# Optimization experiments

Hardware: AMD Instinct MI355X
Metric: run time of the kernel (lower is better)

Reference implementation:

```python
import jax, jax.numpy as jnp
import numpy as np

N_VERT = 100000
N_EDGE = 50000
NNZ = 3200000
IN_CH = 256
OUT_CH = 64


def setup_inputs() -> dict:
    key = jax.random.key(0)
    k1, k2, k3, k4, k5, k6 = jax.random.split(key, 6)
    X = jax.random.normal(k1, (N_VERT, IN_CH), dtype=jnp.float32)
    W = jax.random.normal(k2, (OUT_CH, IN_CH), dtype=jnp.float32) * (IN_CH ** -0.5)
    degE = jax.random.uniform(k3, (N_EDGE,), dtype=jnp.float32, minval=0.01, maxval=1.0)
    degV = jax.random.uniform(k4, (N_VERT,), dtype=jnp.float32, minval=0.01, maxval=1.0)
    Wdiag = jnp.ones((N_EDGE,), dtype=jnp.float32)
    v_idx = jax.random.randint(k5, (NNZ,), 0, N_VERT, dtype=jnp.int32)
    e_idx = jax.random.randint(k6, (NNZ,), 0, N_EDGE, dtype=jnp.int32)
    return {"X": X, "W": W, "degE": degE, "degV": degV, "Wdiag": Wdiag,
            "v_idx": v_idx, "e_idx": e_idx}


def reference(X, W, degE, degV, Wdiag, v_idx, e_idx):
    # Dense projection: [N, in] @ [in, out] -> [N, out]
    Xp = jnp.einsum('ni,oi->no', X, W)
    # Stage 1: vertex -> hyperedge aggregation, degE + Wdiag normalization
    Xe = jax.ops.segment_sum(Xp[v_idx], e_idx, num_segments=N_EDGE)
    Xe = Xe * (degE * Wdiag)[:, None]
    # Stage 2: hyperedge -> vertex aggregation, degV normalization
    Xv = jax.ops.segment_sum(Xe[e_idx], v_idx, num_segments=N_VERT)
    Xv = Xv * degV[:, None]
    return Xv
```

## Files before the change

### kernel.cpp

```cpp
#include <hip/hip_runtime.h>

#define NV   100000
#define NE   50000
#define NNZ  3200000
#define KIN  256
#define KOUT 64

#define NB    256
#define CHUNK (NNZ / NB)
#define TS    6250
#define NBE   782
#define NBV   1563
#define NBINS (NBE + NBV)
#define LSCAN (NBINS * NB)
#define NBLK_SCAN ((LSCAN + 1023) / 1024)

#define PROJ_BLKS 196

#define ECAP_E 6144
#define ECAP_V 4096

typedef short short8 __attribute__((ext_vector_type(8)));
typedef float f32x4  __attribute__((ext_vector_type(4)));

__device__ __forceinline__ unsigned short f2bf(float f) {
    union { float f; unsigned u; } c{f};
    const unsigned lsb = (c.u >> 16) & 1u;
    return (unsigned short)((c.u + 0x7FFFu + lsb) >> 16);
}
__device__ __forceinline__ float bf2f_lo(unsigned u) {
    union { unsigned u; float f; } c{u << 16};
    return c.f;
}
__device__ __forceinline__ float bf2f_hi(unsigned u) {
    union { unsigned u; float f; } c{u & 0xFFFF0000u};
    return c.f;
}
__device__ __forceinline__ short8 pack8(const float4 lo, const float4 hi) {
    short8 r;
    r[0] = (short)f2bf(lo.x); r[1] = (short)f2bf(lo.y);
    r[2] = (short)f2bf(lo.z); r[3] = (short)f2bf(lo.w);
    r[4] = (short)f2bf(hi.x); r[5] = (short)f2bf(hi.y);
    r[6] = (short)f2bf(hi.z); r[7] = (short)f2bf(hi.w);
    return r;
}

__global__ __launch_bounds__(256) void k_wb(const float* __restrict__ W,
                                            unsigned short* __restrict__ Wb) {
    const int i = blockIdx.x * 256 + threadIdx.x;
    Wb[i] = f2bf(W[i]);
}

__global__ __launch_bounds__(1024) void k_projhist(const float* __restrict__ X,
                                                   const unsigned short* __restrict__ Wb,
                                                   unsigned short* __restrict__ Xpb,
                                                   const int* __restrict__ v_idx,
                                                   const int* __restrict__ e_idx,
                                                   int* __restrict__ mat) {
    __shared__ int h[NBINS];
    if (blockIdx.x < PROJ_BLKS) {
        const int tid  = threadIdx.x;
        const int lane = tid & 63;
        const int wv   = tid >> 6;
        const int l15  = lane & 15;
        const int l4   = lane >> 4;
        const int rbase = blockIdx.x * 512 + wv * 32;

        const int r0 = min(rbase + l15,      NV - 1);
        const int r1 = min(rbase + 16 + l15, NV - 1);
        const float* xp0 = X + (size_t)r0 * KIN + l4 * 8;
        const float* xp1 = X + (size_t)r1 * KIN + l4 * 8;
        const unsigned short* wp = Wb + (size_t)l15 * KIN + l4 * 8;

        f32x4 acc[2][4];
#pragma unroll
        for (int t = 0; t < 2; ++t)
#pragma unroll
            for (int g = 0; g < 4; ++g)
                acc[t][g] = (f32x4){0.f, 0.f, 0.f, 0.f};

#pragma unroll
        for (int s = 0; s < 8; ++s) {
            const int k0 = s * 32;
            const float4 a0lo = *(const float4*)(xp0 + k0);
            const float4 a0hi = *(const float4*)(xp0 + k0 + 4);
            const float4 a1lo = *(const float4*)(xp1 + k0);
            const float4 a1hi = *(const float4*)(xp1 + k0 + 4);
            short8 b[4];
#pragma unroll
            for (int g = 0; g < 4; ++g)
                b[g] = *(const short8*)(wp + (size_t)g * 16 * KIN + k0);
            const short8 a0 = pack8(a0lo, a0hi);
            const short8 a1 = pack8(a1lo, a1hi);
#pragma unroll
            for (int g = 0; g < 4; ++g) {
                acc[0][g] = __builtin_amdgcn_mfma_f32_16x16x32_bf16(a0, b[g], acc[0][g], 0, 0, 0);
                acc[1][g] = __builtin_amdgcn_mfma_f32_16x16x32_bf16(a1, b[g], acc[1][g], 0, 0, 0);
            }
        }

#pragma unroll
        for (int t = 0; t < 2; ++t)
#pragma unroll
            for (int i = 0; i < 4; ++i) {
                const int r = rbase + t * 16 + l4 * 4 + i;
                if (r < NV) {
#pragma unroll
                    for (int g = 0; g < 4; ++g)
                        Xpb[(size_t)r * KOUT + g * 16 + l15] = f2bf(acc[t][g][i]);
                }
            }
    } else {
        const int bb = blockIdx.x - PROJ_BLKS;
        const int tid = threadIdx.x;
        for (int i = tid; i < NBINS; i += 1024) h[i] = 0;
        __syncthreads();
        const int base = bb * CHUNK;
        for (int i = tid; i < CHUNK; i += 1024) {
            atomicAdd(&h[e_idx[base + i] >> 6], 1);
            atomicAdd(&h[NBE + (v_idx[base + i] >> 6)], 1);
        }
        __syncthreads();
        for (int j = tid; j < NBINS; j += 1024) mat[j * NB + bb] = h[j];
    }
}

__global__ __launch_bounds__(1024) void k_scan1(int* __restrict__ mat,
                                                int* __restrict__ bsum) {
    __shared__ int buf[1024];
    const int tid = threadIdx.x;
    const int i = blockIdx.x * 1024 + tid;
    const int v = (i < LSCAN) ? mat[i] : 0;
    buf[tid] = v;
    __syncthreads();
    for (int d = 1; d < 1024; d <<= 1) {
        int t = (tid >= d) ? buf[tid - d] : 0;
        __syncthreads();
        buf[tid] += t;
        __syncthreads();
    }
    if (i < LSCAN) mat[i] = buf[tid] - v;
    if (tid == 1023) bsum[blockIdx.x] = buf[1023];
}

__global__ __launch_bounds__(1024) void k_scan2(int* __restrict__ bsum) {
    __shared__ int buf[1024];
    const int tid = threadIdx.x;
    const int v = (tid < NBLK_SCAN) ? bsum[tid] : 0;
    buf[tid] = v;
    __syncthreads();
    for (int d = 1; d < 1024; d <<= 1) {
        int t = (tid >= d) ? buf[tid - d] : 0;
        __syncthreads();
        buf[tid] += t;
        __syncthreads();
    }
    if (tid < NBLK_SCAN) bsum[tid] = buf[tid] - v;
}

__global__ __launch_bounds__(1024) void k_scan3(int* __restrict__ mat,
                                                const int* __restrict__ bsum) {
    const int i = blockIdx.x * 1024 + threadIdx.x;
    if (i < LSCAN) mat[i] += bsum[blockIdx.x];
}

__global__ __launch_bounds__(1024) void k_partsort2(const int* __restrict__ v_idx,
                                                    const int* __restrict__ e_idx,
                                                    const int* __restrict__ mat,
                                                    unsigned* __restrict__ partE,
                                                    unsigned* __restrict__ partV) {
    __shared__ unsigned sbuf[TS];
    __shared__ unsigned short binbuf[TS];
    __shared__ int hist[NBV], pfx[NBV], cur[NBV], gdst[NBV];
    const int side = (blockIdx.x >= NB) ? 1 : 0;
    const int b = blockIdx.x - side * NB;
    const int tid = threadIdx.x;
    const int nbin = side ? NBV : NBE;
    const int rowOff = side ? NBE : 0;
    const int sub    = side ? NNZ : 0;
    unsigned* __restrict__ part = side ? partV : partE;

    for (int j = tid; j < nbin; j += 1024)
        gdst[j] = mat[(rowOff + j) * NB + b] - sub;

    const int base = b * CHUNK;
    for (int tile = 0; tile < CHUNK / TS; ++tile) {
        __syncthreads();
        for (int j = tid; j < nbin; j += 1024) hist[j] = 0;
        __syncthreads();

        int sb[7]; unsigned svv[7];
#pragma unroll
        for (int s = 0; s < 7; ++s) {
            const int li = s * 1024 + tid;
            sb[s] = -1;
            if (li < TS) {
                const int i = base + tile * TS + li;
                const int v = v_idx[i], e = e_idx[i];
                int bin; unsigned val;
                if (side == 0) { bin = e >> 6; val = (unsigned)v | ((unsigned)(e & 63) << 17); }
                else           { bin = v >> 6; val = (unsigned)e | ((unsigned)(v & 63) << 17); }
                atomicAdd(&hist[bin], 1);
                sb[s] = bin; svv[s] = val;
            }
        }
        __syncthreads();

        if (tid < 64) {
            int carry = 0;
            for (int c = 0; c < nbin; c += 64) {
                const int j = c + tid;
                const int h = (j < nbin) ? hist[j] : 0;
                int x = h;
#pragma unroll
                for (int d = 1; d < 64; d <<= 1) {
                    const int y = __shfl_up(x, d, 64);
                    if (tid >= d) x += y;
                }
                if (j < nbin) pfx[j] = carry + x - h;
                carry += __shfl(x, 63, 64);
            }
        }
        __syncthreads();
        for (int j = tid; j < nbin; j += 1024) cur[j] = pfx[j];
        __syncthreads();

#pragma unroll
        for (int s = 0; s < 7; ++s) {
            if (sb[s] >= 0) {
                const int p = atomicAdd(&cur[sb[s]], 1);
                sbuf[p] = svv[s];
                binbuf[p] = (unsigned short)sb[s];
            }
        }
        __syncthreads();

        for (int li = tid; li < TS; li += 1024) {
            const int bin = binbuf[li];
            part[gdst[bin] + (li - pfx[bin])] = sbuf[li];
        }
        __syncthreads();
        for (int j = tid; j < nbin; j += 1024) gdst[j] += cur[j] - pfx[j];
    }
}

__global__ __launch_bounds__(1024) void k_sortgatherE(const unsigned* __restrict__ part,
                                                      const int* __restrict__ mat,
                                                      const unsigned short* __restrict__ Xpb,
                                                      const float* __restrict__ degE,
                                                      const float* __restrict__ Wdiag,
                                                      unsigned short* __restrict__ Xeb) {
    __shared__ unsigned sbuf[ECAP_E];
    __shared__ int hist[64], cur[64], pfx[65];
    const int b = blockIdx.x, tid = threadIdx.x;
    const int base = mat[b * NB];
    const int end  = (b == NBE - 1) ? NNZ : mat[(b + 1) * NB];
    const int nb = end - base;

    if (tid < 64) hist[tid] = 0;
    __syncthreads();
    for (int i = tid; i < nb; i += 1024)
        atomicAdd(&hist[(part[base + i] >> 17) & 63], 1);
    __syncthreads();
    if (tid == 0) {
        int s = 0;
        for (int k = 0; k < 64; ++k) { pfx[k] = s; cur[k] = s; s += hist[k]; }
        pfx[64] = s;
    }
    __syncthreads();
    for (int i = tid; i < nb; i += 1024) {
        const unsigned u = part[base + i];
        const int p = atomicAdd(&cur[(u >> 17) & 63], 1);
        sbuf[p] = u & 0x1FFFFu;
    }
    __syncthreads();

    const int wv = tid >> 6, lane = tid & 63;
    const int q = lane >> 3, sl = lane & 7;
#pragma unroll
    for (int j = 0; j < 4; ++j) {
        const int le = wv * 4 + j;
        const int e_id = (b << 6) + le;
        const int s0 = pfx[le];
        const int n  = pfx[le + 1] - s0;
        float a0 = 0.f, a1 = 0.f, a2 = 0.f, a3 = 0.f,
              a4 = 0.f, a5 = 0.f, a6 = 0.f, a7 = 0.f;
        const int nf = n >> 3;
        int t = 0;
        for (; t + 4 <= nf; t += 4) {
            int idx[4]; uint4 u4[4];
#pragma unroll
            for (int z = 0; z < 4; ++z) idx[z] = (int)sbuf[s0 + 8 * (t + z) + q];
#pragma unroll
            for (int z = 0; z < 4; ++z)
                u4[z] = *(const uint4*)&Xpb[(size_t)idx[z] * KOUT + 8 * sl];
#pragma unroll
            for (int z = 0; z < 4; ++z) {
                a0 += bf2f_lo(u4[z].x); a1 += bf2f_hi(u4[z].x);
                a2 += bf2f_lo(u4[z].y); a3 += bf2f_hi(u4[z].y);
                a4 += bf2f_lo(u4[z].z); a5 += bf2f_hi(u4[z].z);
                a6 += bf2f_lo(u4[z].w); a7 += bf2f_hi(u4[z].w);
            }
        }
        for (; t < nf; ++t) {
            const int idx = (int)sbuf[s0 + 8 * t + q];
            const uint4 u = *(const uint4*)&Xpb[(size_t)idx * KOUT + 8 * sl];
            a0 += bf2f_lo(u.x); a1 += bf2f_hi(u.x);
            a2 += bf2f_lo(u.y); a3 += bf2f_hi(u.y);
            a4 += bf2f_lo(u.z); a5 += bf2f_hi(u.z);
            a6 += bf2f_lo(u.w); a7 += bf2f_hi(u.w);
        }
        if (n & 7) {
            const int src = nf * 8 + q;
            if (src < n) {
                const int idx = (int)sbuf[s0 + src];
                const uint4 u = *(const uint4*)&Xpb[(size_t)idx * KOUT + 8 * sl];
                a0 += bf2f_lo(u.x); a1 += bf2f_hi(u.x);
                a2 += bf2f_lo(u.y); a3 += bf2f_hi(u.y);
                a4 += bf2f_lo(u.z); a5 += bf2f_hi(u.z);
                a6 += bf2f_lo(u.w); a7 += bf2f_hi(u.w);
            }
        }
#pragma unroll
        for (int d = 8; d < 64; d <<= 1) {
            a0 += __shfl_xor(a0, d, 64); a1 += __shfl_xor(a1, d, 64);
            a2 += __shfl_xor(a2, d, 64); a3 += __shfl_xor(a3, d, 64);
            a4 += __shfl_xor(a4, d, 64); a5 += __shfl_xor(a5, d, 64);
            a6 += __shfl_xor(a6, d, 64); a7 += __shfl_xor(a7, d, 64);
        }
        if (q == 0 && e_id < NE) {
            const float s = degE[e_id] * Wdiag[e_id];
            uint4 pk;
            pk.x = (unsigned)f2bf(a0 * s) | ((unsigned)f2bf(a1 * s) << 16);
            pk.y = (unsigned)f2bf(a2 * s) | ((unsigned)f2bf(a3 * s) << 16);
            pk.z = (unsigned)f2bf(a4 * s) | ((unsigned)f2bf(a5 * s) << 16);
            pk.w = (unsigned)f2bf(a6 * s) | ((unsigned)f2bf(a7 * s) << 16);
            *(uint4*)&Xeb[(size_t)e_id * KOUT + 8 * sl] = pk;
        }
    }
}

__global__ __launch_bounds__(1024) void k_sortgatherV(const unsigned* __restrict__ part,
                                                      const int* __restrict__ mat,
                                                      const unsigned short* __restrict__ Xeb,
                                                      const float* __restrict__ degV,
                                                      float* __restrict__ out) {
    __shared__ unsigned sbuf[ECAP_V];
    __shared__ int hist[64], cur[64], pfx[65];
    const int b = blockIdx.x, tid = threadIdx.x;
    const int base = mat[NBE * NB + b * NB] - NNZ;
    const int end  = (b == NBV - 1) ? NNZ : (mat[NBE * NB + (b + 1) * NB] - NNZ);
    const int nb = end - base;

    if (tid < 64) hist[tid] = 0;
    __syncthreads();
    for (int i = tid; i < nb; i += 1024)
        atomicAdd(&hist[(part[base + i] >> 17) & 63], 1);
    __syncthreads();
    if (tid == 0) {
        int s = 0;
        for (int k = 0; k < 64; ++k) { pfx[k] = s; cur[k] = s; s += hist[k]; }
        pfx[64] = s;
    }
    __syncthreads();
    for (int i = tid; i < nb; i += 1024) {
        const unsigned u = part[base + i];
        const int p = atomicAdd(&cur[(u >> 17) & 63], 1);
        sbuf[p] = u & 0x1FFFFu;
    }
    __syncthreads();

    const int wv = tid >> 6, lane = tid & 63;
    const int q = lane >> 3, sl = lane & 7;
#pragma unroll
    for (int j = 0; j < 4; ++j) {
        const int lv = wv * 4 + j;
        const int v_id = (b << 6) + lv;
        const int s0 = pfx[lv];
        const int n  = pfx[lv + 1] - s0;
        float a0 = 0.f, a1 = 0.f, a2 = 0.f, a3 = 0.f,
              a4 = 0.f, a5 = 0.f, a6 = 0.f, a7 = 0.f;
        const int nf = n >> 3;
        int t = 0;
        for (; t + 4 <= nf; t += 4) {
            int idx[4]; uint4 u4[4];
#pragma unroll
            for (int z = 0; z < 4; ++z) idx[z] = (int)sbuf[s0 + 8 * (t + z) + q];
#pragma unroll
            for (int z = 0; z < 4; ++z)
                u4[z] = *(const uint4*)&Xeb[(size_t)idx[z] * KOUT + 8 * sl];
#pragma unroll
            for (int z = 0; z < 4; ++z) {
                a0 += bf2f_lo(u4[z].x); a1 += bf2f_hi(u4[z].x);
                a2 += bf2f_lo(u4[z].y); a3 += bf2f_hi(u4[z].y);
                a4 += bf2f_lo(u4[z].z); a5 += bf2f_hi(u4[z].z);
                a6 += bf2f_lo(u4[z].w); a7 += bf2f_hi(u4[z].w);
            }
        }
        for (; t < nf; ++t) {
            const int idx = (int)sbuf[s0 + 8 * t + q];
            const uint4 u = *(const uint4*)&Xeb[(size_t)idx * KOUT + 8 * sl];
            a0 += bf2f_lo(u.x); a1 += bf2f_hi(u.x);
            a2 += bf2f_lo(u.y); a3 += bf2f_hi(u.y);
            a4 += bf2f_lo(u.z); a5 += bf2f_hi(u.z);
            a6 += bf2f_lo(u.w); a7 += bf2f_hi(u.w);
        }
        if (n & 7) {
            const int src = nf * 8 + q;
            if (src < n) {
                const int idx = (int)sbuf[s0 + src];
                const uint4 u = *(const uint4*)&Xeb[(size_t)idx * KOUT + 8 * sl];
                a0 += bf2f_lo(u.x); a1 += bf2f_hi(u.x);
                a2 += bf2f_lo(u.y); a3 += bf2f_hi(u.y);
                a4 += bf2f_lo(u.z); a5 += bf2f_hi(u.z);
                a6 += bf2f_lo(u.w); a7 += bf2f_hi(u.w);
            }
        }
#pragma unroll
        for (int d = 8; d < 64; d <<= 1) {
            a0 += __shfl_xor(a0, d, 64); a1 += __shfl_xor(a1, d, 64);
            a2 += __shfl_xor(a2, d, 64); a3 += __shfl_xor(a3, d, 64);
            a4 += __shfl_xor(a4, d, 64); a5 += __shfl_xor(a5, d, 64);
            a6 += __shfl_xor(a6, d, 64); a7 += __shfl_xor(a7, d, 64);
        }
        if (q == 0 && v_id < NV) {
            const float s = degV[v_id];
            *(float4*)&out[(size_t)v_id * KOUT + 8 * sl] =
                make_float4(a0 * s, a1 * s, a2 * s, a3 * s);
            *(float4*)&out[(size_t)v_id * KOUT + 8 * sl + 4] =
                make_float4(a4 * s, a5 * s, a6 * s, a7 * s);
        }
    }
}

extern "C" void kernel_launch(void* const* d_in, const int* in_sizes, int n_in,
                              void* d_out, int out_size, void* d_ws, size_t ws_size,
                              hipStream_t stream) {
    const float* X     = (const float*)d_in[0];
    const float* W     = (const float*)d_in[1];
    const float* degE  = (const float*)d_in[2];
    const float* degV  = (const float*)d_in[3];
    const float* Wdiag = (const float*)d_in[4];
    const int*   v_idx = (const int*)d_in[5];
    const int*   e_idx = (const int*)d_in[6];
    float* out = (float*)d_out;

    unsigned short* Xpb  = (unsigned short*)d_ws;
    unsigned short* Xeb  = Xpb + (size_t)NV * KOUT;
    unsigned*       partE = (unsigned*)(Xeb + (size_t)NE * KOUT);
    unsigned*       partV = partE + NNZ;
    int*            mat   = (int*)(partV + NNZ);
    int*            bsum  = mat + LSCAN;
    unsigned short* Wb    = (unsigned short*)(bsum + ((NBLK_SCAN + 3) & ~3));

    k_wb<<<(KIN * KOUT) / 256, 256, 0, stream>>>(W, Wb);

    k_projhist<<<PROJ_BLKS + NB, 1024, 0, stream>>>(X, Wb, Xpb, v_idx, e_idx, mat);

    k_scan1<<<NBLK_SCAN, 1024, 0, stream>>>(mat, bsum);
    k_scan2<<<1, 1024, 0, stream>>>(bsum);
    k_scan3<<<NBLK_SCAN, 1024, 0, stream>>>(mat, bsum);

    k_partsort2<<<2 * NB, 1024, 0, stream>>>(v_idx, e_idx, mat, partE, partV);

    k_sortgatherE<<<NBE, 1024, 0, stream>>>(partE, mat, Xpb, degE, Wdiag, Xeb);
    k_sortgatherV<<<NBV, 1024, 0, stream>>>(partV, mat, Xeb, degV, out);
}
```

Baseline: 207.8 us.

## Spread projection blocks across histogram and scan kernels to fill idle CUs

The 196 projection blocks are split into four groups (80/50/26/40). Each group rides along with one of the histogram, scan1, scan2 and scan3 launches, so projection work fills CUs that the lightly loaded scan kernels leave idle, especially the single-block scan2. This aims to hide the projection GEMM behind the serial scan phases. In exchange, each scan kernel now waits for its projection blocks to finish, and the split ratios are hand-tuned.

```diff
diff --git a/kernel.cpp b/kernel.cpp
--- a/kernel.cpp
+++ b/kernel.cpp
@@ -15,7 +15,10 @@
 #define LSCAN (NBINS * NB)
 #define NBLK_SCAN ((LSCAN + 1023) / 1024)
 
-#define PROJ_BLKS 196
+#define PA 80
+#define PB 50
+#define PC 26
+#define PD 40
 
 #define ECAP_E 6144
 #define ECAP_V 4096
@@ -51,68 +54,74 @@
     Wb[i] = f2bf(W[i]);
 }
 
-__global__ __launch_bounds__(1024) void k_projhist(const float* __restrict__ X,
-                                                   const unsigned short* __restrict__ Wb,
-                                                   unsigned short* __restrict__ Xpb,
-                                                   const int* __restrict__ v_idx,
-                                                   const int* __restrict__ e_idx,
-                                                   int* __restrict__ mat) {
-    __shared__ int h[NBINS];
-    if (blockIdx.x < PROJ_BLKS) {
-        const int tid  = threadIdx.x;
-        const int lane = tid & 63;
-        const int wv   = tid >> 6;
-        const int l15  = lane & 15;
-        const int l4   = lane >> 4;
-        const int rbase = blockIdx.x * 512 + wv * 32;
-
-        const int r0 = min(rbase + l15,      NV - 1);
-        const int r1 = min(rbase + 16 + l15, NV - 1);
-        const float* xp0 = X + (size_t)r0 * KIN + l4 * 8;
-        const float* xp1 = X + (size_t)r1 * KIN + l4 * 8;
-        const unsigned short* wp = Wb + (size_t)l15 * KIN + l4 * 8;
-
-        f32x4 acc[2][4];
-#pragma unroll
-        for (int t = 0; t < 2; ++t)
-#pragma unroll
-            for (int g = 0; g < 4; ++g)
-                acc[t][g] = (f32x4){0.f, 0.f, 0.f, 0.f};
-
-#pragma unroll
-        for (int s = 0; s < 8; ++s) {
-            const int k0 = s * 32;
-            const float4 a0lo = *(const float4*)(xp0 + k0);
-            const float4 a0hi = *(const float4*)(xp0 + k0 + 4);
-            const float4 a1lo = *(const float4*)(xp1 + k0);
-            const float4 a1hi = *(const float4*)(xp1 + k0 + 4);
-            short8 b[4];
-#pragma unroll
-            for (int g = 0; g < 4; ++g)
-                b[g] = *(const short8*)(wp + (size_t)g * 16 * KIN + k0);
-            const short8 a0 = pack8(a0lo, a0hi);
-            const short8 a1 = pack8(a1lo, a1hi);
-#pragma unroll
-            for (int g = 0; g < 4; ++g) {
-                acc[0][g] = __builtin_amdgcn_mfma_f32_16x16x32_bf16(a0, b[g], acc[0][g], 0, 0, 0);
-                acc[1][g] = __builtin_amdgcn_mfma_f32_16x16x32_bf16(a1, b[g], acc[1][g], 0, 0, 0);
-            }
-        }
-
-#pragma unroll
-        for (int t = 0; t < 2; ++t)
-#pragma unroll
-            for (int i = 0; i < 4; ++i) {
-                const int r = rbase + t * 16 + l4 * 4 + i;
-                if (r < NV) {
-#pragma unroll
-                    for (int g = 0; g < 4; ++g)
-                        Xpb[(size_t)r * KOUT + g * 16 + l15] = f2bf(acc[t][g][i]);
-                }
-            }
+__device__ __forceinline__ void proj_body(int pb, int tid,
+                                          const float* __restrict__ X,
+                                          const unsigned short* __restrict__ Wb,
+                                          unsigned short* __restrict__ Xpb) {
+    const int lane = tid & 63;
+    const int wv   = tid >> 6;
+    const int l15  = lane & 15;
+    const int l4   = lane >> 4;
+    const int rbase = pb * 512 + wv * 32;
+
+    const int r0 = min(rbase + l15,      NV - 1);
+    const int r1 = min(rbase + 16 + l15, NV - 1);
+    const float* xp0 = X + (size_t)r0 * KIN + l4 * 8;
+    const float* xp1 = X + (size_t)r1 * KIN + l4 * 8;
+    const unsigned short* wp = Wb + (size_t)l15 * KIN + l4 * 8;
+
+    f32x4 acc[2][4];
+#pragma unroll
+    for (int t = 0; t < 2; ++t)
+#pragma unroll
+        for (int g = 0; g < 4; ++g)
+            acc[t][g] = (f32x4){0.f, 0.f, 0.f, 0.f};
+
+#pragma unroll
+    for (int s = 0; s < 8; ++s) {
+        const int k0 = s * 32;
+        const float4 a0lo = *(const float4*)(xp0 + k0);
+        const float4 a0hi = *(const float4*)(xp0 + k0 + 4);
+        const float4 a1lo = *(const float4*)(xp1 + k0);
+        const float4 a1hi = *(const float4*)(xp1 + k0 + 4);
+        short8 b[4];
+#pragma unroll
+        for (int g = 0; g < 4; ++g)
+            b[g] = *(const short8*)(wp + (size_t)g * 16 * KIN + k0);
+        const short8 a0 = pack8(a0lo, a0hi);
+        const short8 a1 = pack8(a1lo, a1hi);
+#pragma unroll
+        for (int g = 0; g < 4; ++g) {
+            acc[0][g] = __builtin_amdgcn_mfma_f32_16x16x32_bf16(a0, b[g], acc[0][g], 0, 0, 0);
+            acc[1][g] = __builtin_amdgcn_mfma_f32_16x16x32_bf16(a1, b[g], acc[1][g], 0, 0, 0);
+        }
+    }
+
+#pragma unroll
+    for (int t = 0; t < 2; ++t)
+#pragma unroll
+        for (int i = 0; i < 4; ++i) {
+            const int r = rbase + t * 16 + l4 * 4 + i;
+            if (r < NV) {
+#pragma unroll
+                for (int g = 0; g < 4; ++g)
+                    Xpb[(size_t)r * KOUT + g * 16 + l15] = f2bf(acc[t][g][i]);
+            }
+        }
+}
+
+__global__ __launch_bounds__(1024) void k_st1(const float* __restrict__ X,
+                                              const unsigned short* __restrict__ Wb,
+                                              unsigned short* __restrict__ Xpb,
+                                              const int* __restrict__ v_idx,
+                                              const int* __restrict__ e_idx,
+                                              int* __restrict__ mat) {
+    const int tid = threadIdx.x;
+    if (blockIdx.x < PA) {
+        proj_body(blockIdx.x, tid, X, Wb, Xpb);
     } else {
-        const int bb = blockIdx.x - PROJ_BLKS;
-        const int tid = threadIdx.x;
+        __shared__ int h[NBINS];
+        const int bb = blockIdx.x - PA;
         for (int i = tid; i < NBINS; i += 1024) h[i] = 0;
         __syncthreads();
         const int base = bb * CHUNK;
@@ -125,43 +134,67 @@
     }
 }
 
-__global__ __launch_bounds__(1024) void k_scan1(int* __restrict__ mat,
-                                                int* __restrict__ bsum) {
-    __shared__ int buf[1024];
+__global__ __launch_bounds__(1024) void k_st2(const float* __restrict__ X,
+                                              const unsigned short* __restrict__ Wb,
+                                              unsigned short* __restrict__ Xpb,
+                                              int* __restrict__ mat,
+                                              int* __restrict__ bsum) {
     const int tid = threadIdx.x;
-    const int i = blockIdx.x * 1024 + tid;
-    const int v = (i < LSCAN) ? mat[i] : 0;
-    buf[tid] = v;
-    __syncthreads();
-    for (int d = 1; d < 1024; d <<= 1) {
-        int t = (tid >= d) ? buf[tid - d] : 0;
-        __syncthreads();
-        buf[tid] += t;
-        __syncthreads();
-    }
-    if (i < LSCAN) mat[i] = buf[tid] - v;
-    if (tid == 1023) bsum[blockIdx.x] = buf[1023];
-}
-
-__global__ __launch_bounds__(1024) void k_scan2(int* __restrict__ bsum) {
-    __shared__ int buf[1024];
+    if (blockIdx.x < PB) {
+        proj_body(PA + blockIdx.x, tid, X, Wb, Xpb);
+    } else {
+        __shared__ int buf[1024];
+        const int sb = blockIdx.x - PB;
+        const int i = sb * 1024 + tid;
+        const int v = (i < LSCAN) ? mat[i] : 0;
+        buf[tid] = v;
+        __syncthreads();
+        for (int d = 1; d < 1024; d <<= 1) {
+            int t = (tid >= d) ? buf[tid - d] : 0;
+            __syncthreads();
+            buf[tid] += t;
+            __syncthreads();
+        }
+        if (i < LSCAN) mat[i] = buf[tid] - v;
+        if (tid == 1023) bsum[sb] = buf[1023];
+    }
+}
+
+__global__ __launch_bounds__(1024) void k_st3(const float* __restrict__ X,
+                                              const unsigned short* __restrict__ Wb,
+                                              unsigned short* __restrict__ Xpb,
+                                              int* __restrict__ bsum) {
     const int tid = threadIdx.x;
-    const int v = (tid < NBLK_SCAN) ? bsum[tid] : 0;
-    buf[tid] = v;
-    __syncthreads();
-    for (int d = 1; d < 1024; d <<= 1) {
-        int t = (tid >= d) ? buf[tid - d] : 0;
-        __syncthreads();
-        buf[tid] += t;
-        __syncthreads();
-    }
-    if (tid < NBLK_SCAN) bsum[tid] = buf[tid] - v;
-}
-
-__global__ __launch_bounds__(1024) void k_scan3(int* __restrict__ mat,
-                                                const int* __restrict__ bsum) {
-    const int i = blockIdx.x * 1024 + threadIdx.x;
-    if (i < LSCAN) mat[i] += bsum[blockIdx.x];
+    if (blockIdx.x < PC) {
+        proj_body(PA + PB + blockIdx.x, tid, X, Wb, Xpb);
+    } else {
+        __shared__ int buf[1024];
+        const int v = (tid < NBLK_SCAN) ? bsum[tid] : 0;
+        buf[tid] = v;
+        __syncthreads();
+        for (int d = 1; d < 1024; d <<= 1) {
+            int t = (tid >= d) ? buf[tid - d] : 0;
+            __syncthreads();
+            buf[tid] += t;
+            __syncthreads();
+        }
+        if (tid < NBLK_SCAN) bsum[tid] = buf[tid] - v;
+    }
+}
+
+__global__ __launch_bounds__(1024) void k_st4(const float* __restrict__ X,
+                                              const unsigned short* __restrict__ Wb,
+                                              unsigned short* __restrict__ Xpb,
+                                              int* __restrict__ mat,
+                                              const int* __restrict__ bsum) {
+    const int tid = threadIdx.x;
+    if (blockIdx.x < PD) {
+        proj_body(PA + PB + PC + blockIdx.x, tid, X, Wb, Xpb);
+    } else {
+        const int sb = blockIdx.x - PD;
+        const int i = sb * 1024 + tid;
+        if (i < LSCAN) mat[i] += bsum[sb];
+    }
 }
 
 __global__ __launch_bounds__(1024) void k_partsort2(const int* __restrict__ v_idx,
@@ -455,11 +488,10 @@
 
     k_wb<<<(KIN * KOUT) / 256, 256, 0, stream>>>(W, Wb);
 
-    k_projhist<<<PROJ_BLKS + NB, 1024, 0, stream>>>(X, Wb, Xpb, v_idx, e_idx, mat);
-
-    k_scan1<<<NBLK_SCAN, 1024, 0, stream>>>(mat, bsum);
-    k_scan2<<<1, 1024, 0, stream>>>(bsum);
-    k_scan3<<<NBLK_SCAN, 1024, 0, stream>>>(mat, bsum);
+    k_st1<<<PA + NB,        1024, 0, stream>>>(X, Wb, Xpb, v_idx, e_idx, mat);
+    k_st2<<<PB + NBLK_SCAN, 1024, 0, stream>>>(X, Wb, Xpb, mat, bsum);
+    k_st3<<<PC + 1,         1024, 0, stream>>>(X, Wb, Xpb, bsum);
+    k_st4<<<PD + NBLK_SCAN, 1024, 0, stream>>>(X, Wb, Xpb, mat, bsum);
 
     k_partsort2<<<2 * NB, 1024, 0, stream>>>(v_idx, e_idx, mat, partE, partV);
 
```

Result: slower. 280.7 us (+35.1%).
